# Kernel optimization log

Measured on AMD Instinct MI355X. Metric: run time of the kernel, lower is better.

Reference implementation:

```python
import jax, jax.numpy as jnp
import numpy as np
import math

D_MODEL = 768
NUM_HEADS = 8
D_ATT = D_MODEL // NUM_HEADS


def _pos_encoding(S):
    # pe: [S, d_model] sinusoidal, scaled by d_model**-0.5, reshaped to [h, S, d_att]
    position = jnp.arange(S, dtype=jnp.float32)[:, None]                      # [S,1]
    div_term = jnp.exp(jnp.arange(0, D_MODEL, 2, dtype=jnp.float32)
                       * (-math.log(10000.0) / D_MODEL))                      # [d_model/2]
    pe = jnp.zeros((S, D_MODEL), dtype=jnp.float32)
    pe = pe.at[:, 0::2].set(jnp.sin(position * div_term))
    pe = pe.at[:, 1::2].set(jnp.cos(position * div_term))
    pe = pe * (D_MODEL ** -0.5)
    return pe.reshape(S, NUM_HEADS, D_ATT).transpose(1, 0, 2)                 # [h,S,d]


def setup_inputs() -> dict:
    key = jax.random.key(0)
    k1, k2 = jax.random.split(key)
    B, S = 16, 4096
    src = jax.random.normal(k1, (B, S, D_MODEL), dtype=jnp.float32)
    src_key_padding_mask = jnp.zeros((B, S), dtype=bool)  # all valid
    query = jax.random.normal(k2, (NUM_HEADS, D_ATT), dtype=jnp.float32) * (D_ATT ** -0.5)
    return {"src": src, "src_key_padding_mask": src_key_padding_mask, "query": query}


def reference(src, src_key_padding_mask, query):
    B, S, C = src.shape
    key = src.reshape(B, S, NUM_HEADS, D_ATT).transpose(0, 2, 1, 3)          # [B,h,S,d]
    val = key + _pos_encoding(S)[None]                                        # [B,h,S,d]
    scores = jnp.einsum('hd,bhsd->bhs', query, key)                           # [B,h,S]
    scores = jnp.where(src_key_padding_mask[:, None, :], -jnp.inf, scores)
    weights = jax.nn.softmax(scores, axis=-1)                                 # [B,h,S]
    pooled = jnp.einsum('bhsd,bhs->bhd', val, weights)                        # [B,h,d]
    return pooled.reshape(B, NUM_HEADS * D_ATT)                               # [B,C]
```

## Files before the change

### kernel.cpp

```cpp
#include <hip/hip_runtime.h>
#include <math.h>

namespace {
constexpr int kB = 16;
constexpr int kS = 4096;
constexpr int kH = 8;
constexpr int kD = 96;
constexpr int kDM = 768;
constexpr int kNChunk = 16;
constexpr int kCS = kS / kNChunk;
constexpr int kRPI = 32;
constexpr int kIters = kCS / kRPI;
constexpr int kNSC2 = 32;
constexpr int kS2 = kS / kNSC2;
constexpr float kPeScale = 0.03608439182435161f;
constexpr float kNegLog = -9.210340371976184f / 768.0f;
constexpr float kHalfPi = 1.5707963267948966f;
}

__global__ __launch_bounds__(256, 8)
void attn_pass1_kernel(const float* __restrict__ src,
                       const unsigned char* __restrict__ mask,
                       const float* __restrict__ query,
                       float* __restrict__ wsO,
                       float* __restrict__ wsL,
                       float* __restrict__ wsW)
{
    const int blk = blockIdx.x;
    const int chunk = blk & (kNChunk - 1);
    const int bh = blk >> 4;
    const int b = bh >> 3;
    const int h = bh & 7;
    const int t = (int)threadIdx.x;
    const int j = t & 7;
    const int r = t >> 3;
    const int lane = t & 63;
    const int wave = t >> 6;

    const float* qh = query + h * kD + 4 * j;
    const float4 q0 = *(const float4*)(qh);
    const float4 q1 = *(const float4*)(qh + 32);
    const float4 q2 = *(const float4*)(qh + 64);

    float l = 0.0f;
    float o[12];
#pragma unroll
    for (int k = 0; k < 12; ++k) o[k] = 0.0f;

    const int s0 = chunk * kCS + r;
    const float* baseT = src + ((size_t)b * kS + s0) * kDM + h * kD + 4 * j;
    const unsigned char* mbase = mask + (size_t)b * kS + s0;
    float* wbase = wsW + (size_t)bh * kS + s0;

#pragma unroll 1
    for (int it = 0; it < kIters; ++it) {
        const float* rp = baseT + (size_t)(it * kRPI) * kDM;
        const float4 x0 = *(const float4*)(rp);
        const float4 x1 = *(const float4*)(rp + 32);
        const float4 x2 = *(const float4*)(rp + 64);
        const unsigned char mk = mbase[it * kRPI];

        float pd = x0.x * q0.x + x0.y * q0.y + x0.z * q0.z + x0.w * q0.w
                 + x1.x * q1.x + x1.y * q1.y + x1.z * q1.z + x1.w * q1.w
                 + x2.x * q2.x + x2.y * q2.y + x2.z * q2.z + x2.w * q2.w;
        pd += __shfl_xor(pd, 1, 8);
        pd += __shfl_xor(pd, 2, 8);
        pd += __shfl_xor(pd, 4, 8);

        const float w = mk ? 0.0f : __expf(pd);
        l += w;

        o[0]  = fmaf(w, x0.x, o[0]);
        o[1]  = fmaf(w, x0.y, o[1]);
        o[2]  = fmaf(w, x0.z, o[2]);
        o[3]  = fmaf(w, x0.w, o[3]);
        o[4]  = fmaf(w, x1.x, o[4]);
        o[5]  = fmaf(w, x1.y, o[5]);
        o[6]  = fmaf(w, x1.z, o[6]);
        o[7]  = fmaf(w, x1.w, o[7]);
        o[8]  = fmaf(w, x2.x, o[8]);
        o[9]  = fmaf(w, x2.y, o[9]);
        o[10] = fmaf(w, x2.z, o[10]);
        o[11] = fmaf(w, x2.w, o[11]);

        if (j == 0) wbase[it * kRPI] = w;
    }

    __shared__ float ssum[4];
    __shared__ float osh[4][8][12];

    float lv = (j == 0) ? l : 0.0f;
#pragma unroll
    for (int msk = 32; msk >= 1; msk >>= 1) lv += __shfl_xor(lv, msk, 64);
    if (lane == 0) ssum[wave] = lv;

#pragma unroll
    for (int k = 0; k < 12; ++k) {
        float v = o[k];
        v += __shfl_xor(v, 8, 64);
        v += __shfl_xor(v, 16, 64);
        v += __shfl_xor(v, 32, 64);
        o[k] = v;
    }
    if (lane < 8) {
#pragma unroll
        for (int k = 0; k < 12; ++k) osh[wave][lane][k] = o[k];
    }
    __syncthreads();

    const int pidx = bh * kNChunk + chunk;
    if (t < kD) {
        const int kk = t >> 5;
        const int jj = (t & 31) >> 2;
        const int qq = t & 3;
        const int idx = kk * 4 + qq;
        wsO[(size_t)pidx * kD + t] = osh[0][jj][idx] + osh[1][jj][idx]
                                   + osh[2][jj][idx] + osh[3][jj][idx];
    }
    if (t == 0) {
        wsL[pidx] = ssum[0] + ssum[1] + ssum[2] + ssum[3];
    }
}

__global__ __launch_bounds__(128)
void attn_pe_kernel(const float* __restrict__ wsW, float* __restrict__ wsP)
{
    const int blk = (int)blockIdx.x;
    const int sc = blk & (kNSC2 - 1);
    const int bh = blk >> 5;
    const int h = bh & 7;
    const int c = (int)threadIdx.x;
    if (c >= kD) return;

    const float f = __expf(kNegLog * (float)(h * kD + (c & ~1)));
    const int s0 = sc * kS2;
    float sn, cs;
    __sincosf((float)s0 * f + ((c & 1) ? kHalfPi : 0.0f), &sn, &cs);
    float ds, dc;
    __sincosf(f, &ds, &dc);

    const float* wp = wsW + (size_t)bh * kS + s0;
    float acc = 0.0f;
#pragma unroll 4
    for (int i = 0; i < kS2; ++i) {
        const float w = wp[i];
        acc = fmaf(w, sn, acc);
        const float ns = fmaf(sn, dc, cs * ds);
        const float nc = fmaf(cs, dc, -sn * ds);
        sn = ns; cs = nc;
    }
    wsP[(size_t)blk * kD + c] = acc * kPeScale;
}

__global__ __launch_bounds__(128)
void attn_combine_kernel(const float* __restrict__ wsO,
                         const float* __restrict__ wsL,
                         const float* __restrict__ wsP,
                         float* __restrict__ out)
{
    const int bh = (int)blockIdx.x;
    const int t = (int)threadIdx.x;

    float L = 0.0f;
#pragma unroll
    for (int k = 0; k < kNChunk; ++k) L += wsL[bh * kNChunk + k];

    if (t < kD) {
        float acc = 0.0f;
#pragma unroll
        for (int k = 0; k < kNChunk; ++k)
            acc += wsO[(size_t)(bh * kNChunk + k) * kD + t];
#pragma unroll
        for (int k = 0; k < kNSC2; ++k)
            acc += wsP[(size_t)(bh * kNSC2 + k) * kD + t];
        out[(size_t)bh * kD + t] = acc / L;
    }
}

extern "C" void kernel_launch(void* const* d_in, const int* in_sizes, int n_in,
                              void* d_out, int out_size, void* d_ws, size_t ws_size,
                              hipStream_t stream)
{
    const float* src = (const float*)d_in[0];
    const unsigned char* mask = (const unsigned char*)d_in[1];
    const float* query = (const float*)d_in[2];
    float* out = (float*)d_out;

    float* wsO = (float*)d_ws;
    float* wsL = wsO + (size_t)kB * kH * kNChunk * kD;
    float* wsW = wsL + (size_t)kB * kH * kNChunk;
    float* wsP = wsW + (size_t)kB * kH * kS;

    hipLaunchKernelGGL(attn_pass1_kernel,
                       dim3(kB * kH * kNChunk), dim3(256), 0, stream,
                       src, mask, query, wsO, wsL, wsW);
    hipLaunchKernelGGL(attn_pe_kernel,
                       dim3(kB * kH * kNSC2), dim3(128), 0, stream,
                       wsW, wsP);
    hipLaunchKernelGGL(attn_combine_kernel,
                       dim3(kB * kH), dim3(128), 0, stream,
                       wsO, wsL, wsP, out);
}
```

Measured before the change: 292.1 us.

## Process full rows per wave across all heads with register prefetch

New measurement: 298.1 us. +2.1%, slower.

```diff
diff --git a/kernel.cpp b/kernel.cpp
--- a/kernel.cpp
+++ b/kernel.cpp
@@ -7,10 +7,9 @@
 constexpr int kH = 8;
 constexpr int kD = 96;
 constexpr int kDM = 768;
-constexpr int kNChunk = 16;
-constexpr int kCS = kS / kNChunk;
-constexpr int kRPI = 32;
-constexpr int kIters = kCS / kRPI;
+constexpr int kNC = 64;
+constexpr int kCS = kS / kNC;
+constexpr int kRW = kCS / 4;
 constexpr int kNSC2 = 32;
 constexpr int kS2 = kS / kNSC2;
 constexpr float kPeScale = 0.03608439182435161f;
@@ -18,47 +17,52 @@
 constexpr float kHalfPi = 1.5707963267948966f;
 }
 
-__global__ __launch_bounds__(256, 8)
-void attn_pass1_kernel(const float* __restrict__ src,
-                       const unsigned char* __restrict__ mask,
-                       const float* __restrict__ query,
-                       float* __restrict__ wsO,
-                       float* __restrict__ wsL,
-                       float* __restrict__ wsW)
-{
-    const int blk = blockIdx.x;
-    const int chunk = blk & (kNChunk - 1);
-    const int bh = blk >> 4;
-    const int b = bh >> 3;
-    const int h = bh & 7;
+__global__ __launch_bounds__(256)
+void attn_pass1(const float* __restrict__ src,
+                const unsigned char* __restrict__ mask,
+                const float* __restrict__ query,
+                float* __restrict__ wsO,
+                float* __restrict__ wsL,
+                float* __restrict__ wsW)
+{
+    const int blk = (int)blockIdx.x;
+    const int b = blk >> 6;
+    const int chunk = blk & (kNC - 1);
     const int t = (int)threadIdx.x;
-    const int j = t & 7;
-    const int r = t >> 3;
+    const int wave = t >> 6;
     const int lane = t & 63;
-    const int wave = t >> 6;
-
-    const float* qh = query + h * kD + 4 * j;
-    const float4 q0 = *(const float4*)(qh);
-    const float4 q1 = *(const float4*)(qh + 32);
-    const float4 q2 = *(const float4*)(qh + 64);
+    const int h = lane >> 3;
+
+    const float* qf = query + 12 * lane;
+    const float4 q0 = *(const float4*)(qf);
+    const float4 q1 = *(const float4*)(qf + 4);
+    const float4 q2 = *(const float4*)(qf + 8);
 
     float l = 0.0f;
     float o[12];
 #pragma unroll
     for (int k = 0; k < 12; ++k) o[k] = 0.0f;
 
-    const int s0 = chunk * kCS + r;
-    const float* baseT = src + ((size_t)b * kS + s0) * kDM + h * kD + 4 * j;
-    const unsigned char* mbase = mask + (size_t)b * kS + s0;
-    float* wbase = wsW + (size_t)bh * kS + s0;
-
-#pragma unroll 1
-    for (int it = 0; it < kIters; ++it) {
-        const float* rp = baseT + (size_t)(it * kRPI) * kDM;
-        const float4 x0 = *(const float4*)(rp);
-        const float4 x1 = *(const float4*)(rp + 32);
-        const float4 x2 = *(const float4*)(rp + 64);
-        const unsigned char mk = mbase[it * kRPI];
+    const int s0 = chunk * kCS + wave;
+    const float* base = src + ((size_t)b * kS + s0) * kDM + 12 * lane;
+    const unsigned char* mb = mask + (size_t)b * kS + s0;
+    float* wb = wsW + ((size_t)b * kS + s0) * kH + h;
+
+    float4 x0 = *(const float4*)(base);
+    float4 x1 = *(const float4*)(base + 4);
+    float4 x2 = *(const float4*)(base + 8);
+    unsigned char mk = mb[0];
+
+    for (int it = 0; it < kRW; ++it) {
+        float4 nx0 = {}, nx1 = {}, nx2 = {};
+        unsigned char nmk = 0;
+        if (it + 1 < kRW) {
+            const float* np = base + (size_t)((it + 1) * 4) * kDM;
+            nx0 = *(const float4*)(np);
+            nx1 = *(const float4*)(np + 4);
+            nx2 = *(const float4*)(np + 8);
+            nmk = mb[(it + 1) * 4];
+        }
 
         float pd = x0.x * q0.x + x0.y * q0.y + x0.z * q0.z + x0.w * q0.w
                  + x1.x * q1.x + x1.y * q1.y + x1.z * q1.z + x1.w * q1.w
@@ -83,51 +87,45 @@
         o[10] = fmaf(w, x2.z, o[10]);
         o[11] = fmaf(w, x2.w, o[11]);
 
-        if (j == 0) wbase[it * kRPI] = w;
-    }
-
-    __shared__ float ssum[4];
-    __shared__ float osh[4][8][12];
-
-    float lv = (j == 0) ? l : 0.0f;
-#pragma unroll
-    for (int msk = 32; msk >= 1; msk >>= 1) lv += __shfl_xor(lv, msk, 64);
-    if (lane == 0) ssum[wave] = lv;
-
-#pragma unroll
-    for (int k = 0; k < 12; ++k) {
-        float v = o[k];
-        v += __shfl_xor(v, 8, 64);
-        v += __shfl_xor(v, 16, 64);
-        v += __shfl_xor(v, 32, 64);
-        o[k] = v;
-    }
-    if (lane < 8) {
-#pragma unroll
-        for (int k = 0; k < 12; ++k) osh[wave][lane][k] = o[k];
-    }
+        if ((lane & 7) == 0) wb[(size_t)(it * 4) * kH] = w;
+
+        x0 = nx0; x1 = nx1; x2 = nx2; mk = nmk;
+    }
+
+    __shared__ float osum[4][kDM];
+    __shared__ float lsum[4][kH];
+
+    float* op = &osum[wave][12 * lane];
+    ((float4*)op)[0] = make_float4(o[0], o[1], o[2], o[3]);
+    ((float4*)op)[1] = make_float4(o[4], o[5], o[6], o[7]);
+    ((float4*)op)[2] = make_float4(o[8], o[9], o[10], o[11]);
+    if ((lane & 7) == 0) lsum[wave][h] = l;
     __syncthreads();
 
-    const int pidx = bh * kNChunk + chunk;
-    if (t < kD) {
-        const int kk = t >> 5;
-        const int jj = (t & 31) >> 2;
-        const int qq = t & 3;
-        const int idx = kk * 4 + qq;
-        wsO[(size_t)pidx * kD + t] = osh[0][jj][idx] + osh[1][jj][idx]
-                                   + osh[2][jj][idx] + osh[3][jj][idx];
-    }
-    if (t == 0) {
-        wsL[pidx] = ssum[0] + ssum[1] + ssum[2] + ssum[3];
+    if (t < kDM / 4) {
+        const float4 a0 = ((const float4*)&osum[0][0])[t];
+        const float4 a1 = ((const float4*)&osum[1][0])[t];
+        const float4 a2 = ((const float4*)&osum[2][0])[t];
+        const float4 a3 = ((const float4*)&osum[3][0])[t];
+        float4 r;
+        r.x = a0.x + a1.x + a2.x + a3.x;
+        r.y = a0.y + a1.y + a2.y + a3.y;
+        r.z = a0.z + a1.z + a2.z + a3.z;
+        r.w = a0.w + a1.w + a2.w + a3.w;
+        ((float4*)(wsO + (size_t)blk * kDM))[t] = r;
+    }
+    if (t < kH) {
+        wsL[blk * kH + t] = lsum[0][t] + lsum[1][t] + lsum[2][t] + lsum[3][t];
     }
 }
 
 __global__ __launch_bounds__(128)
-void attn_pe_kernel(const float* __restrict__ wsW, float* __restrict__ wsP)
+void attn_pe(const float* __restrict__ wsW, float* __restrict__ wsP)
 {
     const int blk = (int)blockIdx.x;
     const int sc = blk & (kNSC2 - 1);
     const int bh = blk >> 5;
+    const int b = bh >> 3;
     const int h = bh & 7;
     const int c = (int)threadIdx.x;
     if (c >= kD) return;
@@ -139,11 +137,11 @@
     float ds, dc;
     __sincosf(f, &ds, &dc);
 
-    const float* wp = wsW + (size_t)bh * kS + s0;
+    const float* wp = wsW + ((size_t)b * kS + s0) * kH + h;
     float acc = 0.0f;
 #pragma unroll 4
     for (int i = 0; i < kS2; ++i) {
-        const float w = wp[i];
+        const float w = wp[(size_t)i * kH];
         acc = fmaf(w, sn, acc);
         const float ns = fmaf(sn, dc, cs * ds);
         const float nc = fmaf(cs, dc, -sn * ds);
@@ -153,26 +151,28 @@
 }
 
 __global__ __launch_bounds__(128)
-void attn_combine_kernel(const float* __restrict__ wsO,
-                         const float* __restrict__ wsL,
-                         const float* __restrict__ wsP,
-                         float* __restrict__ out)
+void attn_combine(const float* __restrict__ wsO,
+                  const float* __restrict__ wsL,
+                  const float* __restrict__ wsP,
+                  float* __restrict__ out)
 {
     const int bh = (int)blockIdx.x;
+    const int b = bh >> 3;
+    const int h = bh & 7;
     const int t = (int)threadIdx.x;
 
     float L = 0.0f;
 #pragma unroll
-    for (int k = 0; k < kNChunk; ++k) L += wsL[bh * kNChunk + k];
+    for (int cc = 0; cc < kNC; ++cc) L += wsL[(b * kNC + cc) * kH + h];
 
     if (t < kD) {
         float acc = 0.0f;
-#pragma unroll
-        for (int k = 0; k < kNChunk; ++k)
-            acc += wsO[(size_t)(bh * kNChunk + k) * kD + t];
-#pragma unroll
-        for (int k = 0; k < kNSC2; ++k)
-            acc += wsP[(size_t)(bh * kNSC2 + k) * kD + t];
+#pragma unroll 8
+        for (int cc = 0; cc < kNC; ++cc)
+            acc += wsO[(size_t)(b * kNC + cc) * kDM + h * kD + t];
+#pragma unroll 8
+        for (int sc = 0; sc < kNSC2; ++sc)
+            acc += wsP[(size_t)(bh * kNSC2 + sc) * kD + t];
         out[(size_t)bh * kD + t] = acc / L;
     }
 }
@@ -187,17 +187,17 @@
     float* out = (float*)d_out;
 
     float* wsO = (float*)d_ws;
-    float* wsL = wsO + (size_t)kB * kH * kNChunk * kD;
-    float* wsW = wsL + (size_t)kB * kH * kNChunk;
-    float* wsP = wsW + (size_t)kB * kH * kS;
-
-    hipLaunchKernelGGL(attn_pass1_kernel,
-                       dim3(kB * kH * kNChunk), dim3(256), 0, stream,
+    float* wsL = wsO + (size_t)kB * kNC * kDM;
+    float* wsW = wsL + (size_t)kB * kNC * kH;
+    float* wsP = wsW + (size_t)kB * kS * kH;
+
+    hipLaunchKernelGGL(attn_pass1,
+                       dim3(kB * kNC), dim3(256), 0, stream,
                        src, mask, query, wsO, wsL, wsW);
-    hipLaunchKernelGGL(attn_pe_kernel,
+    hipLaunchKernelGGL(attn_pe,
                        dim3(kB * kH * kNSC2), dim3(128), 0, stream,
                        wsW, wsP);
-    hipLaunchKernelGGL(attn_combine_kernel,
+    hipLaunchKernelGGL(attn_combine,
                        dim3(kB * kH), dim3(128), 0, stream,
                        wsO, wsL, wsP, out);
 }
```
